# Optimization experiments

Hardware: AMD Instinct MI355X
Metric: run time of the kernel (lower is better)

## Reference

```python
import jax, jax.numpy as jnp
import numpy as np

EPS = 1e-5  # flax BatchNorm default epsilon


def setup_inputs() -> dict:
    key = jax.random.key(0)
    ks = jax.random.split(key, 4)
    E, D, H = 6400000, 12, 12
    N = 100000
    return {
        "edges": jax.random.normal(ks[0], (E, D), dtype=jnp.float32),
        "bn_scale": jnp.ones((D,), jnp.float32),
        "bn_bias": jnp.zeros((D,), jnp.float32),
        "bn_mean": jnp.zeros((D,), jnp.float32),
        "bn_var": jnp.ones((D,), jnp.float32),
        "W1": jax.random.normal(ks[1], (D, H), dtype=jnp.float32) / np.sqrt(D),
        "b1": jnp.zeros((H,), jnp.float32),
        "W2": jax.random.normal(ks[2], (H, H), dtype=jnp.float32) / np.sqrt(H),
        "b2": jnp.zeros((H,), jnp.float32),
        "receivers": jax.random.randint(ks[3], (E,), 0, N, dtype=jnp.int32),
        "num_nodes": N,
    }


def reference(edges, bn_scale, bn_bias, bn_mean, bn_var, W1, b1, W2, b2, receivers, num_nodes):
    # EdgeEncoder (eval mode): BatchNorm(running stats) -> Dense(12) -> ReLU -> Dense(12)
    x = (edges - bn_mean) * (bn_scale * jax.lax.rsqrt(bn_var + EPS)) + bn_bias
    x = jax.nn.relu(x @ W1 + b1)
    x = x @ W2 + b2  # [E, 12] per-edge messages
    # aggregate messages into receiver nodes (update_node_fn returns this directly)
    nodes = jax.ops.segment_sum(x, receivers, num_segments=num_nodes)  # [N, 12]
    return nodes
```

## Files before the change

kernel.cpp:

```cpp
#include <hip/hip_runtime.h>

#define D      12
#define ASTR   13
#define LOGNPB 7
#define NPB    128
#define CAP    9216
#define EPB    16384
#define ABLK   256
#define SBLK   256
#define CBLK   256
#define SPLIT  2

#define SWZ(p) ((p) ^ (((p) >> 5) & 31))

__global__ __launch_bounds__(ABLK) void passA_hist(
    const int* __restrict__ receivers, long E, int nbuck,
    int* __restrict__ cnt )
{
    extern __shared__ int hist[];
    for (int i = threadIdx.x; i < nbuck; i += ABLK) hist[i] = 0;
    __syncthreads();
    long e0 = (long)blockIdx.x * EPB;
    long e1 = e0 + EPB; if (e1 > E) e1 = E;
    for (long e = e0 + threadIdx.x; e < e1; e += ABLK) {
        int r = receivers[e];
        atomicAdd(&hist[r >> LOGNPB], 1);
    }
    __syncthreads();
    int* row = cnt + (long)blockIdx.x * nbuck;
    for (int i = threadIdx.x; i < nbuck; i += ABLK) row[i] = hist[i];
}

__global__ __launch_bounds__(SBLK) void passS1_colscan(
    int* __restrict__ cnt, int nblk, int nbuck, int* __restrict__ totals)
{
    int b = blockIdx.x;
    int t = threadIdx.x;
    __shared__ int csum[SBLK];
    int per = (nblk + SBLK - 1) / SBLK;
    int i0 = t * per;
    int i1 = i0 + per; if (i1 > nblk) i1 = nblk;
    int s = 0;
    for (int i = i0; i < i1; ++i) s += cnt[(long)i * nbuck + b];
    csum[t] = s;
    __syncthreads();
    for (int off = 1; off < SBLK; off <<= 1) {
        int add = (t >= off) ? csum[t - off] : 0;
        __syncthreads();
        csum[t] += add;
        __syncthreads();
    }
    int run = csum[t] - s;
    for (int i = i0; i < i1; ++i) {
        long a = (long)i * nbuck + b;
        int tmp = cnt[a];
        cnt[a] = run;
        run += tmp;
    }
    if (t == SBLK - 1) totals[b] = csum[SBLK - 1];
}

__global__ __launch_bounds__(1024) void passS2_basescan(
    const int* __restrict__ totals, int* __restrict__ base, int nbuck)
{
    __shared__ int sh[1024];
    int t = threadIdx.x;
    int v = (t < nbuck) ? totals[t] : 0;
    sh[t] = v;
    __syncthreads();
    for (int off = 1; off < 1024; off <<= 1) {
        int add = (t >= off) ? sh[t - off] : 0;
        __syncthreads();
        sh[t] += add;
        __syncthreads();
    }
    if (t < nbuck) base[t] = sh[t] - v;
}

__global__ __launch_bounds__(ABLK) void passB_scatter(
    const int* __restrict__ receivers, long E, int nbuck,
    const int* __restrict__ cnt, const int* __restrict__ base,
    unsigned int* __restrict__ sorted)
{
    extern __shared__ int cur[];
    const int* row = cnt + (long)blockIdx.x * nbuck;
    for (int i = threadIdx.x; i < nbuck; i += ABLK) cur[i] = row[i] + base[i];
    __syncthreads();
    long e0 = (long)blockIdx.x * EPB;
    long e1 = e0 + EPB; if (e1 > E) e1 = E;
    for (long e = e0 + threadIdx.x; e < e1; e += ABLK) {
        int r = receivers[e];
        int b = r >> LOGNPB;
        int pos = atomicAdd(&cur[b], 1);
        sorted[pos] = ((unsigned)e << LOGNPB) | (unsigned)(r & (NPB - 1));
    }
}

__device__ __forceinline__ void build_weights(
    int t,
    const float* __restrict__ bn_scale, const float* __restrict__ bn_bias,
    const float* __restrict__ bn_mean,  const float* __restrict__ bn_var,
    const float* __restrict__ W1, const float* __restrict__ b1,
    const float* __restrict__ W2, const float* __restrict__ b2,
    float* sW1, float* sW2, float* sB1, float* sB2)
{
    if (t < D * D) {
        int d = t / D;
        float a = bn_scale[d] * rsqrtf(bn_var[d] + 1e-5f);
        sW1[t] = a * W1[t];
        sW2[t] = W2[t];
    }
    if (t < D) {
        float acc = b1[t];
        #pragma unroll
        for (int d = 0; d < D; ++d) {
            float a = bn_scale[d] * rsqrtf(bn_var[d] + 1e-5f);
            float c = bn_bias[d] - bn_mean[d] * a;
            acc += c * W1[d * D + t];
        }
        sB1[t] = acc;
        sB2[t] = b2[t];
    }
}

__device__ __forceinline__ void mlp12(
    const float x[D],
    const float* sW1, const float* sW2, const float* sB1, const float* sB2,
    float y[D])
{
    float h[D];
    #pragma unroll
    for (int j = 0; j < D; ++j) h[j] = sB1[j];
    #pragma unroll
    for (int d = 0; d < D; ++d) {
        float xd = x[d];
        #pragma unroll
        for (int j = 0; j < D; ++j) h[j] = fmaf(xd, sW1[d * D + j], h[j]);
    }
    #pragma unroll
    for (int j = 0; j < D; ++j) h[j] = fmaxf(h[j], 0.f);
    #pragma unroll
    for (int j = 0; j < D; ++j) y[j] = sB2[j];
    #pragma unroll
    for (int d = 0; d < D; ++d) {
        float hd = h[d];
        #pragma unroll
        for (int j = 0; j < D; ++j) y[j] = fmaf(hd, sW2[d * D + j], y[j]);
    }
}

__global__ __launch_bounds__(CBLK) void passC_nodesort(
    const float* __restrict__ edges,
    const unsigned int* __restrict__ sortedG,
    const int* __restrict__ base, const int* __restrict__ totals,
    const float* __restrict__ bn_scale, const float* __restrict__ bn_bias,
    const float* __restrict__ bn_mean,  const float* __restrict__ bn_var,
    const float* __restrict__ W1, const float* __restrict__ b1,
    const float* __restrict__ W2, const float* __restrict__ b2,
    float* __restrict__ part,
    float* __restrict__ out,
    long total , long slab )
{
    __shared__ float sW1[D * D], sW2[D * D], sB1[D], sB2[D];
    __shared__ int hist[NPB];
    __shared__ int off[NPB + 1];
    __shared__ int cur[NPB];
    __shared__ unsigned sorted2[CAP];
    __shared__ float facc[NPB * ASTR];

    const int t = threadIdx.x;
    build_weights(t, bn_scale, bn_bias, bn_mean, bn_var, W1, b1, W2, b2,
                  sW1, sW2, sB1, sB2);
    for (int i = t; i < NPB * ASTR; i += CBLK) facc[i] = 0.f;
    if (t < NPB) hist[t] = 0;
    __syncthreads();

    const int b = blockIdx.x;
    const int s = blockIdx.y;
    const int S = gridDim.y;
    const int s0 = base[b];
    const int n  = totals[b];
    const int chunk = (n + S - 1) / S;
    const int g0 = s * chunk;
    int g1 = g0 + chunk; if (g1 > n) g1 = n;
    const int ns = g1 - g0;
    const unsigned* __restrict__ src = sortedG + s0 + g0;

    if (ns > 0 && ns <= CAP) {
        for (int k = t; k < ns; k += CBLK)
            atomicAdd(&hist[src[k] & (NPB - 1)], 1);
        __syncthreads();

        int myh = (t < NPB) ? hist[t] : 0;
        if (t < NPB) off[t] = myh;
        __syncthreads();
        for (int d2 = 1; d2 < NPB; d2 <<= 1) {
            int add = 0;
            if (t < NPB && t >= d2) add = off[t - d2];
            __syncthreads();
            if (t < NPB) off[t] += add;
            __syncthreads();
        }
        if (t < NPB) cur[t] = off[t] - myh;
        __syncthreads();
        if (t < NPB) off[t] = cur[t];
        if (t == 0) off[NPB] = ns;
        __syncthreads();

        for (int k = t; k < ns; k += CBLK) {
            unsigned e = src[k];
            int pos = atomicAdd(&cur[e & (NPB - 1)], 1);
            sorted2[SWZ(pos)] = e >> LOGNPB;
        }
        __syncthreads();

        const int per = (ns + CBLK - 1) / CBLK;
        int k0 = t * per;
        int k1 = k0 + per; if (k1 > ns) k1 = ns;
        if (k0 < k1) {
            int cu = 0;
            while (off[cu + 1] <= k0) ++cu;
            int nodeEnd = off[cu + 1];

            float ac[D];
            #pragma unroll
            for (int j = 0; j < D; ++j) ac[j] = 0.f;

            auto edge_mlp = [&](float4 c0, float4 c1, float4 c2) {
                float x[D] = {c0.x, c0.y, c0.z, c0.w, c1.x, c1.y, c1.z, c1.w,
                              c2.x, c2.y, c2.z, c2.w};
                float h[D];
                #pragma unroll
                for (int j = 0; j < D; ++j) h[j] = sB1[j];
                #pragma unroll
                for (int d = 0; d < D; ++d) {
                    float xd = x[d];
                    #pragma unroll
                    for (int j = 0; j < D; ++j) h[j] = fmaf(xd, sW1[d * D + j], h[j]);
                }
                #pragma unroll
                for (int j = 0; j < D; ++j) h[j] = fmaxf(h[j], 0.f);
                #pragma unroll
                for (int d = 0; d < D; ++d) {
                    float hd = h[d];
                    #pragma unroll
                    for (int j = 0; j < D; ++j) ac[j] = fmaf(hd, sW2[d * D + j], ac[j]);
                }
            };

            const int kL = k1 - 1;
            unsigned iA = sorted2[SWZ(k0)];
            unsigned iB = sorted2[SWZ((k0 + 1 <= kL) ? k0 + 1 : kL)];
            const float4* pA = reinterpret_cast<const float4*>(edges + (long)iA * D);
            const float4* pB = reinterpret_cast<const float4*>(edges + (long)iB * D);
            float4 a0 = pA[0], a1 = pA[1], a2 = pA[2];
            float4 b0 = pB[0], b1v = pB[1], b2v = pB[2];

            for (int k = k0; k < k1; k += 2) {
                int kn0 = (k + 2 <= kL) ? k + 2 : kL;
                int kn1 = (k + 3 <= kL) ? k + 3 : kL;
                unsigned jA = sorted2[SWZ(kn0)];
                unsigned jB = sorted2[SWZ(kn1)];
                const float4* qA = reinterpret_cast<const float4*>(edges + (long)jA * D);
                const float4* qB = reinterpret_cast<const float4*>(edges + (long)jB * D);
                float4 na0 = qA[0], na1 = qA[1], na2 = qA[2];
                float4 nb0 = qB[0], nb1 = qB[1], nb2 = qB[2];

                if (k >= nodeEnd) {
                    #pragma unroll
                    for (int j = 0; j < D; ++j) {
                        atomicAdd(&facc[cu * ASTR + j], ac[j]);
                        ac[j] = 0.f;
                    }
                    do { ++cu; } while (off[cu + 1] <= k);
                    nodeEnd = off[cu + 1];
                }
                edge_mlp(a0, a1, a2);

                if (k + 1 < k1) {
                    if (k + 1 >= nodeEnd) {
                        #pragma unroll
                        for (int j = 0; j < D; ++j) {
                            atomicAdd(&facc[cu * ASTR + j], ac[j]);
                            ac[j] = 0.f;
                        }
                        do { ++cu; } while (off[cu + 1] <= k + 1);
                        nodeEnd = off[cu + 1];
                    }
                    edge_mlp(b0, b1v, b2v);
                }
                a0 = na0; a1 = na1; a2 = na2;
                b0 = nb0; b1v = nb1; b2v = nb2;
            }
            #pragma unroll
            for (int j = 0; j < D; ++j) atomicAdd(&facc[cu * ASTR + j], ac[j]);
        }
    } else if (ns > 0) {
        for (int k = t; k < ns; k += CBLK) {
            unsigned e = src[k];
            const float4* p = reinterpret_cast<const float4*>(edges + (long)(e >> LOGNPB) * D);
            float4 c0 = p[0], c1 = p[1], c2 = p[2];
            float x[D] = {c0.x, c0.y, c0.z, c0.w, c1.x, c1.y, c1.z, c1.w,
                          c2.x, c2.y, c2.z, c2.w};
            float y[D];
            mlp12(x, sW1, sW2, sB1, sB2, y);
            int rloc = (int)(e & (NPB - 1));
            #pragma unroll
            for (int j = 0; j < D; ++j) atomicAdd(&facc[rloc * ASTR + j], y[j]);
        }
    }
    __syncthreads();

    if (part != nullptr) {
        float* dst = part + (long)s * slab + (long)b * (NPB * D);
        for (int i = t; i < NPB * D; i += CBLK) {
            int node = i / D, j = i % D;
            dst[i] = facc[node * ASTR + j] + (float)hist[node] * sB2[j];
        }
    } else {
        long obase = (long)b * (NPB * D);
        long cnt_w = total - obase; if (cnt_w > NPB * D) cnt_w = NPB * D;
        for (long i = t; i < cnt_w; i += CBLK) {
            int node = (int)i / D, j = (int)i % D;
            out[obase + i] = facc[node * ASTR + j] + (float)hist[node] * sB2[j];
        }
    }
}

__global__ __launch_bounds__(CBLK) void reduce_partials(
    const float* __restrict__ part, float* __restrict__ out,
    long total4, long slab4, int S)
{
    long i = (long)blockIdx.x * CBLK + threadIdx.x;
    if (i >= total4) return;
    const float4* p = reinterpret_cast<const float4*>(part);
    float4 v = p[i];
    for (int s = 1; s < S; ++s) {
        float4 w = p[(long)s * slab4 + i];
        v.x += w.x; v.y += w.y; v.z += w.z; v.w += w.w;
    }
    reinterpret_cast<float4*>(out)[i] = v;
}

#define EPT 4
__global__ __launch_bounds__(ABLK) void edge_mlp_scatter(
    const float* __restrict__ edges,
    const float* __restrict__ bn_scale, const float* __restrict__ bn_bias,
    const float* __restrict__ bn_mean,  const float* __restrict__ bn_var,
    const float* __restrict__ W1, const float* __restrict__ b1,
    const float* __restrict__ W2, const float* __restrict__ b2,
    const int* __restrict__ receivers, float* __restrict__ out, long E)
{
    __shared__ float sW1[D * D], sW2[D * D], sB1[D], sB2[D];
    const int t = threadIdx.x;
    build_weights(t, bn_scale, bn_bias, bn_mean, bn_var, W1, b1, W2, b2,
                  sW1, sW2, sB1, sB2);
    __syncthreads();
    const long basee = (long)blockIdx.x * (ABLK * EPT) + t;
    #pragma unroll
    for (int kk = 0; kk < EPT; ++kk) {
        long e = basee + (long)kk * ABLK;
        if (e >= E) continue;
        int r = receivers[e];
        const float4* p = reinterpret_cast<const float4*>(edges + e * D);
        float4 v0 = p[0], v1 = p[1], v2 = p[2];
        float x[D] = {v0.x, v0.y, v0.z, v0.w, v1.x, v1.y, v1.z, v1.w,
                      v2.x, v2.y, v2.z, v2.w};
        float y[D];
        mlp12(x, sW1, sW2, sB1, sB2, y);
        #pragma unroll
        for (int j = 0; j < D; ++j) atomicAdd(&out[(long)r * D + j], y[j]);
    }
}

extern "C" void kernel_launch(void* const* d_in, const int* in_sizes, int n_in,
                              void* d_out, int out_size, void* d_ws, size_t ws_size,
                              hipStream_t stream) {
    const float* edges     = (const float*)d_in[0];
    const float* bn_scale  = (const float*)d_in[1];
    const float* bn_bias   = (const float*)d_in[2];
    const float* bn_mean   = (const float*)d_in[3];
    const float* bn_var    = (const float*)d_in[4];
    const float* W1        = (const float*)d_in[5];
    const float* b1        = (const float*)d_in[6];
    const float* W2        = (const float*)d_in[7];
    const float* b2        = (const float*)d_in[8];
    const int*   receivers = (const int*)d_in[9];
    float*       out       = (float*)d_out;

    const long E = (long)in_sizes[0] / D;
    const int  N = out_size / D;

    const int  nbuck = (N + NPB - 1) >> LOGNPB;
    const long nblk  = (E + EPB - 1) / EPB;
    const size_t cntBytes  = (size_t)nblk * (size_t)nbuck * 4u;
    const size_t slabBytes = (size_t)nbuck * (size_t)(NPB * D) * 4u;
    const size_t baseNeed  = cntBytes + 2u * (size_t)nbuck * 4u + (size_t)E * 4u + 512u;
    const size_t fullNeed  = baseNeed + (size_t)SPLIT * slabBytes + 256u;
    const long total = (long)N * D;

    const bool shapeOK = (nbuck <= 1024) && (E < (1L << 25));

    if (shapeOK && ws_size >= baseNeed) {
        const int S = (ws_size >= fullNeed) ? SPLIT : 1;

        char* w = (char*)d_ws;
        int* cnt    = (int*)w;  w += cntBytes;
        int* totals = (int*)w;  w += (size_t)nbuck * 4u;
        int* basep  = (int*)w;  w += (size_t)nbuck * 4u;
        unsigned int* sortedG = (unsigned int*)w;  w += (size_t)E * 4u;
        float* part = (S > 1) ? (float*)(((uintptr_t)w + 255u) & ~(uintptr_t)255u) : nullptr;

        const size_t lds = (size_t)nbuck * 4u;
        const long slab = (long)nbuck * (NPB * D);

        passA_hist    <<<dim3((unsigned)nblk), dim3(ABLK), lds, stream>>>(receivers, E, nbuck, cnt);
        passS1_colscan<<<dim3((unsigned)nbuck), dim3(SBLK), 0, stream>>>(cnt, (int)nblk, nbuck, totals);
        passS2_basescan<<<dim3(1), dim3(1024), 0, stream>>>(totals, basep, nbuck);
        passB_scatter <<<dim3((unsigned)nblk), dim3(ABLK), lds, stream>>>(receivers, E, nbuck, cnt, basep, sortedG);
        passC_nodesort<<<dim3((unsigned)nbuck, (unsigned)S), dim3(CBLK), 0, stream>>>(
            edges, sortedG, basep, totals,
            bn_scale, bn_bias, bn_mean, bn_var, W1, b1, W2, b2,
            part, out, total, slab);
        if (S > 1) {
            const long total4 = total / 4;
            const long rblocks = (total4 + CBLK - 1) / CBLK;
            reduce_partials<<<dim3((unsigned)rblocks), dim3(CBLK), 0, stream>>>(
                part, out, total4, slab / 4, S);
        }
        return;
    }

    (void)hipMemsetAsync(d_out, 0, (size_t)out_size * sizeof(float), stream);
    const long blocks = (E + (long)(ABLK * EPT) - 1) / (long)(ABLK * EPT);
    edge_mlp_scatter<<<dim3((unsigned)blocks), dim3(ABLK), 0, stream>>>(
        edges, bn_scale, bn_bias, bn_mean, bn_var, W1, b1, W2, b2,
        receivers, out, E);
}
```

Baseline: 397.7 us.

## Convert edge features to bf16 before gathered per-node MLP accumulation

Adds a pre-pass that converts the fp32 edge matrix to a packed bf16 copy in workspace, so the random row gathers in the node-sorted pass read 24 bytes per edge instead of 48. The split pass now uses a smaller LDS sort buffer and a single-edge prefetch loop, and a separate fp32 path covers smaller workspaces. The extra conversion pass streams the full edge array and writes half as much, so the gain depends on the gather traffic it saves outweighing that. Rounding inputs to bf16 also reduces accuracy.

```diff
diff --git a/kernel.cpp b/kernel.cpp
--- a/kernel.cpp
+++ b/kernel.cpp
@@ -4,7 +4,8 @@
 #define ASTR   13
 #define LOGNPB 7
 #define NPB    128
-#define CAP    9216
+#define CAPBF  5120
+#define CAPF   9216
 #define EPB    16384
 #define ABLK   256
 #define SBLK   256
@@ -12,6 +13,40 @@
 #define SPLIT  2
 
 #define SWZ(p) ((p) ^ (((p) >> 5) & 31))
+
+static __device__ __forceinline__ unsigned f2bf(float f) {
+    union { float f; unsigned u; } v; v.f = f;
+    unsigned r = v.u + 0x7FFFu + ((v.u >> 16) & 1u);
+    return r >> 16;
+}
+static __device__ __forceinline__ float bf_lo(unsigned u) {
+    union { unsigned u; float f; } v; v.u = u << 16; return v.f;
+}
+static __device__ __forceinline__ float bf_hi(unsigned u) {
+    union { unsigned u; float f; } v; v.u = u & 0xFFFF0000u; return v.f;
+}
+
+__global__ __launch_bounds__(256) void cvt_bf16(
+    const float* __restrict__ in, unsigned* __restrict__ outw,
+    long n8 , long ntot )
+{
+    long i = (long)blockIdx.x * 256 + threadIdx.x;
+    const long stride = (long)gridDim.x * 256;
+    for (; i < n8; i += stride) {
+        const float4* p = reinterpret_cast<const float4*>(in + i * 8);
+        float4 a = p[0], b = p[1];
+        uint4 w;
+        w.x = f2bf(a.x) | (f2bf(a.y) << 16);
+        w.y = f2bf(a.z) | (f2bf(a.w) << 16);
+        w.z = f2bf(b.x) | (f2bf(b.y) << 16);
+        w.w = f2bf(b.z) | (f2bf(b.w) << 16);
+        reinterpret_cast<uint4*>(outw)[i] = w;
+    }
+    if (blockIdx.x == 0 && threadIdx.x == 0) {
+        for (long j = n8 * 8; j < ntot; ++j)
+            reinterpret_cast<unsigned short*>(outw)[j] = (unsigned short)f2bf(in[j]);
+    }
+}
 
 __global__ __launch_bounds__(ABLK) void passA_hist(
     const int* __restrict__ receivers, long E, int nbuck,
@@ -149,8 +184,8 @@
     }
 }
 
-__global__ __launch_bounds__(CBLK) void passC_nodesort(
-    const float* __restrict__ edges,
+__global__ __launch_bounds__(CBLK) void passC_bf(
+    const uint2* __restrict__ bfrows,
     const unsigned int* __restrict__ sortedG,
     const int* __restrict__ base, const int* __restrict__ totals,
     const float* __restrict__ bn_scale, const float* __restrict__ bn_bias,
@@ -165,7 +200,7 @@
     __shared__ int hist[NPB];
     __shared__ int off[NPB + 1];
     __shared__ int cur[NPB];
-    __shared__ unsigned sorted2[CAP];
+    __shared__ unsigned sorted2[CAPBF];
     __shared__ float facc[NPB * ASTR];
 
     const int t = threadIdx.x;
@@ -186,7 +221,7 @@
     const int ns = g1 - g0;
     const unsigned* __restrict__ src = sortedG + s0 + g0;
 
-    if (ns > 0 && ns <= CAP) {
+    if (ns > 0 && ns <= CAPBF) {
         for (int k = t; k < ns; k += CBLK)
             atomicAdd(&hist[src[k] & (NPB - 1)], 1);
         __syncthreads();
@@ -226,9 +261,30 @@
             #pragma unroll
             for (int j = 0; j < D; ++j) ac[j] = 0.f;
 
-            auto edge_mlp = [&](float4 c0, float4 c1, float4 c2) {
-                float x[D] = {c0.x, c0.y, c0.z, c0.w, c1.x, c1.y, c1.z, c1.w,
-                              c2.x, c2.y, c2.z, c2.w};
+            const int kmax = k1 - 1;
+            unsigned idx = sorted2[SWZ(k0)];
+            const uint2* rp = bfrows + (size_t)idx * 3;
+            uint2 r0 = rp[0], r1 = rp[1], r2 = rp[2];
+
+            for (int k = k0; k < k1; ++k) {
+                int kn = (k + 1 <= kmax) ? k + 1 : kmax;
+                unsigned nidx = sorted2[SWZ(kn)];
+                const uint2* q = bfrows + (size_t)nidx * 3;
+                uint2 n0 = q[0], n1 = q[1], n2 = q[2];
+
+                if (k >= nodeEnd) {
+                    #pragma unroll
+                    for (int j = 0; j < D; ++j) {
+                        atomicAdd(&facc[cu * ASTR + j], ac[j]);
+                        ac[j] = 0.f;
+                    }
+                    do { ++cu; } while (off[cu + 1] <= k);
+                    nodeEnd = off[cu + 1];
+                }
+
+                float x[D] = {bf_lo(r0.x), bf_hi(r0.x), bf_lo(r0.y), bf_hi(r0.y),
+                              bf_lo(r1.x), bf_hi(r1.x), bf_lo(r1.y), bf_hi(r1.y),
+                              bf_lo(r2.x), bf_hi(r2.x), bf_lo(r2.y), bf_hi(r2.y)};
                 float h[D];
                 #pragma unroll
                 for (int j = 0; j < D; ++j) h[j] = sB1[j];
@@ -246,26 +302,133 @@
                     #pragma unroll
                     for (int j = 0; j < D; ++j) ac[j] = fmaf(hd, sW2[d * D + j], ac[j]);
                 }
-            };
-
-            const int kL = k1 - 1;
-            unsigned iA = sorted2[SWZ(k0)];
-            unsigned iB = sorted2[SWZ((k0 + 1 <= kL) ? k0 + 1 : kL)];
-            const float4* pA = reinterpret_cast<const float4*>(edges + (long)iA * D);
-            const float4* pB = reinterpret_cast<const float4*>(edges + (long)iB * D);
-            float4 a0 = pA[0], a1 = pA[1], a2 = pA[2];
-            float4 b0 = pB[0], b1v = pB[1], b2v = pB[2];
-
-            for (int k = k0; k < k1; k += 2) {
-                int kn0 = (k + 2 <= kL) ? k + 2 : kL;
-                int kn1 = (k + 3 <= kL) ? k + 3 : kL;
-                unsigned jA = sorted2[SWZ(kn0)];
-                unsigned jB = sorted2[SWZ(kn1)];
-                const float4* qA = reinterpret_cast<const float4*>(edges + (long)jA * D);
-                const float4* qB = reinterpret_cast<const float4*>(edges + (long)jB * D);
-                float4 na0 = qA[0], na1 = qA[1], na2 = qA[2];
-                float4 nb0 = qB[0], nb1 = qB[1], nb2 = qB[2];
-
+                r0 = n0; r1 = n1; r2 = n2;
+            }
+            #pragma unroll
+            for (int j = 0; j < D; ++j) atomicAdd(&facc[cu * ASTR + j], ac[j]);
+        }
+    } else if (ns > 0) {
+        for (int k = t; k < ns; k += CBLK) {
+            unsigned e = src[k];
+            const uint2* rp = bfrows + (size_t)(e >> LOGNPB) * 3;
+            uint2 r0 = rp[0], r1 = rp[1], r2 = rp[2];
+            float x[D] = {bf_lo(r0.x), bf_hi(r0.x), bf_lo(r0.y), bf_hi(r0.y),
+                          bf_lo(r1.x), bf_hi(r1.x), bf_lo(r1.y), bf_hi(r1.y),
+                          bf_lo(r2.x), bf_hi(r2.x), bf_lo(r2.y), bf_hi(r2.y)};
+            float y[D];
+            mlp12(x, sW1, sW2, sB1, sB2, y);
+            int rloc = (int)(e & (NPB - 1));
+            #pragma unroll
+            for (int j = 0; j < D; ++j) atomicAdd(&facc[rloc * ASTR + j], y[j]);
+        }
+    }
+    __syncthreads();
+
+    if (part != nullptr) {
+        float* dst = part + (long)s * slab + (long)b * (NPB * D);
+        for (int i = t; i < NPB * D; i += CBLK) {
+            int node = i / D, j = i % D;
+            dst[i] = facc[node * ASTR + j] + (float)hist[node] * sB2[j];
+        }
+    } else {
+        long obase = (long)b * (NPB * D);
+        long cnt_w = total - obase; if (cnt_w > NPB * D) cnt_w = NPB * D;
+        for (long i = t; i < cnt_w; i += CBLK) {
+            int node = (int)i / D, j = (int)i % D;
+            out[obase + i] = facc[node * ASTR + j] + (float)hist[node] * sB2[j];
+        }
+    }
+}
+
+__global__ __launch_bounds__(CBLK) void reduce_partials(
+    const float* __restrict__ part, float* __restrict__ out,
+    long total4, long slab4, int S)
+{
+    long i = (long)blockIdx.x * CBLK + threadIdx.x;
+    if (i >= total4) return;
+    const float4* p = reinterpret_cast<const float4*>(part);
+    float4 v = p[i];
+    for (int s = 1; s < S; ++s) {
+        float4 w = p[(long)s * slab4 + i];
+        v.x += w.x; v.y += w.y; v.z += w.z; v.w += w.w;
+    }
+    reinterpret_cast<float4*>(out)[i] = v;
+}
+
+__global__ __launch_bounds__(CBLK) void passC_f32(
+    const float* __restrict__ edges,
+    const unsigned int* __restrict__ sortedG,
+    const int* __restrict__ base, const int* __restrict__ totals,
+    const float* __restrict__ bn_scale, const float* __restrict__ bn_bias,
+    const float* __restrict__ bn_mean,  const float* __restrict__ bn_var,
+    const float* __restrict__ W1, const float* __restrict__ b1,
+    const float* __restrict__ W2, const float* __restrict__ b2,
+    float* __restrict__ out, long total)
+{
+    __shared__ float sW1[D * D], sW2[D * D], sB1[D], sB2[D];
+    __shared__ int hist[NPB];
+    __shared__ int off[NPB + 1];
+    __shared__ int cur[NPB];
+    __shared__ unsigned sorted2[CAPF];
+    __shared__ float facc[NPB * ASTR];
+
+    const int t = threadIdx.x;
+    build_weights(t, bn_scale, bn_bias, bn_mean, bn_var, W1, b1, W2, b2,
+                  sW1, sW2, sB1, sB2);
+    for (int i = t; i < NPB * ASTR; i += CBLK) facc[i] = 0.f;
+    if (t < NPB) hist[t] = 0;
+    __syncthreads();
+
+    const int b = blockIdx.x;
+    const int s0 = base[b];
+    const int n  = totals[b];
+
+    if (n <= CAPF) {
+        for (int k = t; k < n; k += CBLK)
+            atomicAdd(&hist[sortedG[s0 + k] & (NPB - 1)], 1);
+        __syncthreads();
+        int myh = (t < NPB) ? hist[t] : 0;
+        if (t < NPB) off[t] = myh;
+        __syncthreads();
+        for (int d2 = 1; d2 < NPB; d2 <<= 1) {
+            int add = 0;
+            if (t < NPB && t >= d2) add = off[t - d2];
+            __syncthreads();
+            if (t < NPB) off[t] += add;
+            __syncthreads();
+        }
+        if (t < NPB) cur[t] = off[t] - myh;
+        __syncthreads();
+        if (t < NPB) off[t] = cur[t];
+        if (t == 0) off[NPB] = n;
+        __syncthreads();
+        for (int k = t; k < n; k += CBLK) {
+            unsigned e = sortedG[s0 + k];
+            int pos = atomicAdd(&cur[e & (NPB - 1)], 1);
+            sorted2[SWZ(pos)] = e >> LOGNPB;
+        }
+        __syncthreads();
+
+        const int per = (n + CBLK - 1) / CBLK;
+        int k0 = t * per;
+        int k1 = k0 + per; if (k1 > n) k1 = n;
+        if (k0 < k1) {
+            int cu = 0;
+            while (off[cu + 1] <= k0) ++cu;
+            int nodeEnd = off[cu + 1];
+            float ac[D];
+            #pragma unroll
+            for (int j = 0; j < D; ++j) ac[j] = 0.f;
+            unsigned idx = sorted2[SWZ(k0)];
+            const float4* p = reinterpret_cast<const float4*>(edges + (long)idx * D);
+            float4 c0 = p[0], c1 = p[1], c2 = p[2];
+            for (int k = k0; k < k1; ++k) {
+                float4 n0 = c0, n1 = c1, n2 = c2;
+                if (k + 1 < k1) {
+                    unsigned ix = sorted2[SWZ(k + 1)];
+                    const float4* q = reinterpret_cast<const float4*>(edges + (long)ix * D);
+                    n0 = q[0]; n1 = q[1]; n2 = q[2];
+                }
                 if (k >= nodeEnd) {
                     #pragma unroll
                     for (int j = 0; j < D; ++j) {
@@ -275,29 +438,20 @@
                     do { ++cu; } while (off[cu + 1] <= k);
                     nodeEnd = off[cu + 1];
                 }
-                edge_mlp(a0, a1, a2);
-
-                if (k + 1 < k1) {
-                    if (k + 1 >= nodeEnd) {
-                        #pragma unroll
-                        for (int j = 0; j < D; ++j) {
-                            atomicAdd(&facc[cu * ASTR + j], ac[j]);
-                            ac[j] = 0.f;
-                        }
-                        do { ++cu; } while (off[cu + 1] <= k + 1);
-                        nodeEnd = off[cu + 1];
-                    }
-                    edge_mlp(b0, b1v, b2v);
-                }
-                a0 = na0; a1 = na1; a2 = na2;
-                b0 = nb0; b1v = nb1; b2v = nb2;
+                float x[D] = {c0.x, c0.y, c0.z, c0.w, c1.x, c1.y, c1.z, c1.w,
+                              c2.x, c2.y, c2.z, c2.w};
+                float y[D];
+                mlp12(x, sW1, sW2, sB1, sB2, y);
+                #pragma unroll
+                for (int j = 0; j < D; ++j) ac[j] += y[j];
+                c0 = n0; c1 = n1; c2 = n2;
             }
             #pragma unroll
             for (int j = 0; j < D; ++j) atomicAdd(&facc[cu * ASTR + j], ac[j]);
         }
-    } else if (ns > 0) {
-        for (int k = t; k < ns; k += CBLK) {
-            unsigned e = src[k];
+    } else {
+        for (int k = t; k < n; k += CBLK) {
+            unsigned e = sortedG[s0 + k];
             const float4* p = reinterpret_cast<const float4*>(edges + (long)(e >> LOGNPB) * D);
             float4 c0 = p[0], c1 = p[1], c2 = p[2];
             float x[D] = {c0.x, c0.y, c0.z, c0.w, c1.x, c1.y, c1.z, c1.w,
@@ -311,35 +465,10 @@
     }
     __syncthreads();
 
-    if (part != nullptr) {
-        float* dst = part + (long)s * slab + (long)b * (NPB * D);
-        for (int i = t; i < NPB * D; i += CBLK) {
-            int node = i / D, j = i % D;
-            dst[i] = facc[node * ASTR + j] + (float)hist[node] * sB2[j];
-        }
-    } else {
-        long obase = (long)b * (NPB * D);
-        long cnt_w = total - obase; if (cnt_w > NPB * D) cnt_w = NPB * D;
-        for (long i = t; i < cnt_w; i += CBLK) {
-            int node = (int)i / D, j = (int)i % D;
-            out[obase + i] = facc[node * ASTR + j] + (float)hist[node] * sB2[j];
-        }
-    }
-}
-
-__global__ __launch_bounds__(CBLK) void reduce_partials(
-    const float* __restrict__ part, float* __restrict__ out,
-    long total4, long slab4, int S)
-{
-    long i = (long)blockIdx.x * CBLK + threadIdx.x;
-    if (i >= total4) return;
-    const float4* p = reinterpret_cast<const float4*>(part);
-    float4 v = p[i];
-    for (int s = 1; s < S; ++s) {
-        float4 w = p[(long)s * slab4 + i];
-        v.x += w.x; v.y += w.y; v.z += w.z; v.w += w.w;
-    }
-    reinterpret_cast<float4*>(out)[i] = v;
+    long obase = (long)b * (NPB * D);
+    long cnt_w = total - obase; if (cnt_w > NPB * D) cnt_w = NPB * D;
+    for (long i = t; i < cnt_w; i += CBLK)
+        out[obase + i] = facc[((int)i / D) * ASTR + ((int)i % D)];
 }
 
 #define EPT 4
@@ -394,40 +523,60 @@
     const int  nbuck = (N + NPB - 1) >> LOGNPB;
     const long nblk  = (E + EPB - 1) / EPB;
     const size_t cntBytes  = (size_t)nblk * (size_t)nbuck * 4u;
+    const size_t head      = cntBytes + 2u * (size_t)nbuck * 4u + 512u;
+    const size_t bfBytes   = (size_t)E * 24u;
     const size_t slabBytes = (size_t)nbuck * (size_t)(NPB * D) * 4u;
-    const size_t baseNeed  = cntBytes + 2u * (size_t)nbuck * 4u + (size_t)E * 4u + 512u;
-    const size_t fullNeed  = baseNeed + (size_t)SPLIT * slabBytes + 256u;
+    const size_t needT1 = head + (size_t)E * 4u + bfBytes + (size_t)SPLIT * slabBytes + 1024u;
+    const size_t needT2 = head + (size_t)E * 4u;
     const long total = (long)N * D;
 
     const bool shapeOK = (nbuck <= 1024) && (E < (1L << 25));
-
-    if (shapeOK && ws_size >= baseNeed) {
-        const int S = (ws_size >= fullNeed) ? SPLIT : 1;
-
+    const size_t lds = (size_t)nbuck * 4u;
+
+    if (shapeOK && ws_size >= needT1) {
         char* w = (char*)d_ws;
         int* cnt    = (int*)w;  w += cntBytes;
         int* totals = (int*)w;  w += (size_t)nbuck * 4u;
         int* basep  = (int*)w;  w += (size_t)nbuck * 4u;
         unsigned int* sortedG = (unsigned int*)w;  w += (size_t)E * 4u;
-        float* part = (S > 1) ? (float*)(((uintptr_t)w + 255u) & ~(uintptr_t)255u) : nullptr;
-
-        const size_t lds = (size_t)nbuck * 4u;
-        const long slab = (long)nbuck * (NPB * D);
-
+        unsigned* bfw = (unsigned*)(((uintptr_t)w + 255u) & ~(uintptr_t)255u);
+        w = (char*)bfw + bfBytes;
+        float* part = (float*)(((uintptr_t)w + 255u) & ~(uintptr_t)255u);
+
+        const long ntot = E * D;
+        const long n8 = ntot / 8;
+        cvt_bf16      <<<dim3(2048), dim3(256), 0, stream>>>(edges, bfw, n8, ntot);
         passA_hist    <<<dim3((unsigned)nblk), dim3(ABLK), lds, stream>>>(receivers, E, nbuck, cnt);
         passS1_colscan<<<dim3((unsigned)nbuck), dim3(SBLK), 0, stream>>>(cnt, (int)nblk, nbuck, totals);
         passS2_basescan<<<dim3(1), dim3(1024), 0, stream>>>(totals, basep, nbuck);
         passB_scatter <<<dim3((unsigned)nblk), dim3(ABLK), lds, stream>>>(receivers, E, nbuck, cnt, basep, sortedG);
-        passC_nodesort<<<dim3((unsigned)nbuck, (unsigned)S), dim3(CBLK), 0, stream>>>(
-            edges, sortedG, basep, totals,
+
+        const long slab = (long)nbuck * (NPB * D);
+        passC_bf      <<<dim3((unsigned)nbuck, SPLIT), dim3(CBLK), 0, stream>>>(
+            (const uint2*)bfw, sortedG, basep, totals,
             bn_scale, bn_bias, bn_mean, bn_var, W1, b1, W2, b2,
             part, out, total, slab);
-        if (S > 1) {
-            const long total4 = total / 4;
-            const long rblocks = (total4 + CBLK - 1) / CBLK;
-            reduce_partials<<<dim3((unsigned)rblocks), dim3(CBLK), 0, stream>>>(
-                part, out, total4, slab / 4, S);
-        }
+        const long total4 = total / 4;
+        const long rblocks = (total4 + CBLK - 1) / CBLK;
+        reduce_partials<<<dim3((unsigned)rblocks), dim3(CBLK), 0, stream>>>(
+            part, out, total4, slab / 4, SPLIT);
+        return;
+    }
+
+    if (shapeOK && ws_size >= needT2) {
+        char* w = (char*)d_ws;
+        int* cnt    = (int*)w;  w += cntBytes;
+        int* totals = (int*)w;  w += (size_t)nbuck * 4u;
+        int* basep  = (int*)w;  w += (size_t)nbuck * 4u;
+        unsigned int* sortedG = (unsigned int*)w;
+
+        passA_hist    <<<dim3((unsigned)nblk), dim3(ABLK), lds, stream>>>(receivers, E, nbuck, cnt);
+        passS1_colscan<<<dim3((unsigned)nbuck), dim3(SBLK), 0, stream>>>(cnt, (int)nblk, nbuck, totals);
+        passS2_basescan<<<dim3(1), dim3(1024), 0, stream>>>(totals, basep, nbuck);
+        passB_scatter <<<dim3((unsigned)nblk), dim3(ABLK), lds, stream>>>(receivers, E, nbuck, cnt, basep, sortedG);
+        passC_f32     <<<dim3((unsigned)nbuck), dim3(CBLK), 0, stream>>>(
+            edges, sortedG, basep, totals,
+            bn_scale, bn_bias, bn_mean, bn_var, W1, b1, W2, b2, out, total);
         return;
     }
 
```

Measured after the change: 427.4 us. +7.5%, slower.
